# Optimization experiments

Hardware: AMD Instinct MI355X
Metric: run time of the kernel (lower is better)

## Reference

```python
import jax, jax.numpy as jnp
import numpy as np
from jax import lax

KS = 7  # kernel-prediction footprint at 1/4 res
DN = ('NCHW', 'OIHW', 'NCHW')


def _conv(x, W, b):
    y = lax.conv_general_dilated(x, W, (1, 1), 'VALID', dimension_numbers=DN)
    return y + b[None, :, None, None]


def _apply_kernels(kernel, data, ks):
    # kernel: [bs, ks*ks, kh, kw]; data: [bs, 1, h, w]
    kh, kw = kernel.shape[2], kernel.shape[3]
    h, w = data.shape[2], data.shape[3]
    ch = (h - (kh + ks - 1)) // 2
    cw = (w - (kw + ks - 1)) // 2
    if ch > 0:
        data = data[:, :, ch:h - ch, :]
    if cw > 0:
        data = data[:, :, :, cw:w - cw]
    # patches: [bs, ks*ks, kh, kw], flat tap index = dy*ks+dx (row-major), same as torch unfold+view
    patches = lax.conv_general_dilated_patches(data, (ks, ks), (1, 1), 'VALID')
    return jnp.sum(kernel * patches, axis=1, keepdims=True)


def _crop_like(a, b):
    dh = (a.shape[2] - b.shape[2]) // 2
    dw = (a.shape[3] - b.shape[3]) // 2
    if dh > 0 or dw > 0:
        a = a[:, :, dh:a.shape[2] - dh, dw:a.shape[3] - dw]
    return a


def _unroll(buf):
    # [bs,4,h,w] quarter-res -> [bs,1,2h,2w] full-res (channel c=2p+q -> offset (p,q))
    bs, _, h, w = buf.shape
    return buf.reshape(bs, 2, 2, h, w).transpose(0, 3, 1, 4, 2).reshape(bs, 1, 2 * h, 2 * w)


def reference(mosaic, W0, b0, W1, b1, W2, b2, W3, b3, W4, b4):
    gray = mosaic.sum(axis=1)  # [bs,H,W]
    # GRBG 2x2 phase extraction, matching torch unfold(2,2,2).unfold(1,2,2).permute(0,3,4,1,2)
    g0 = gray[:, 0::2, 0::2][:, None]
    b_ = gray[:, 1::2, 0::2][:, None]
    r = gray[:, 0::2, 1::2][:, None]
    g1 = gray[:, 1::2, 1::2][:, None]
    x = jnp.concatenate([g0, b_, r, g1], axis=1)  # [bs,4,h,w]

    # ConvChain: 5 valid 3x3 convs, relu on all but last (linear output)
    for (W, bb) in ((W0, b0), (W1, b1), (W2, b2), (W3, b3)):
        x = jax.nn.relu(_conv(x, W, bb))
    kernels = _conv(x, W4, b4)  # [bs, 10*KS*KS, kh, kw]

    k2 = KS * KS
    idx = 0

    reds = [r]
    for _ in range(3):
        k = jax.nn.softmax(kernels[:, idx:idx + k2], axis=1)
        idx += k2
        reds.append(_apply_kernels(k, r, KS))
    reds[0] = _crop_like(reds[0], reds[1])
    red = _unroll(jnp.concatenate([reds[1], reds[0], reds[2], reds[3]], axis=1))

    blues = [b_]
    for _ in range(3):
        k = jax.nn.softmax(kernels[:, idx:idx + k2], axis=1)
        idx += k2
        blues.append(_apply_kernels(k, b_, KS))
    blues[0] = _crop_like(blues[0], blues[1])
    blue = _unroll(jnp.concatenate([blues[1], blues[2], blues[0], blues[3]], axis=1))

    greens = [g0, g1]
    for _ in range(2):
        k = jax.nn.softmax(kernels[:, idx:idx + 2 * k2], axis=1)
        idx += 2 * k2
        greens.append(_apply_kernels(k[:, :k2], g0, KS) + _apply_kernels(k[:, k2:], g1, KS))
    greens[0] = _crop_like(greens[0], greens[2])
    greens[1] = _crop_like(greens[1], greens[2])
    green = _unroll(jnp.concatenate([greens[0], greens[2], greens[3], greens[1]], axis=1))

    return jnp.concatenate([red, green, blue], axis=1)  # [bs,3,2*kh,2*kw]


def setup_inputs() -> dict:
    key = jax.random.key(0)
    ks = jax.random.split(key, 6)
    bs, H, W = 2, 768, 768
    mosaic = jax.random.uniform(ks[0], (bs, 3, H, W), dtype=jnp.float32)

    def w(k, o, i):
        return jax.random.normal(k, (o, i, 3, 3), jnp.float32) * (1.0 / np.sqrt(i * 9))

    z = lambda n: jnp.zeros((n,), jnp.float32)
    return {
        'mosaic': mosaic,
        'W0': w(ks[1], 64, 4), 'b0': z(64),
        'W1': w(ks[2], 64, 64), 'b1': z(64),
        'W2': w(ks[3], 64, 64), 'b2': z(64),
        'W3': w(ks[4], 64, 64), 'b3': z(64),
        'W4': w(ks[5], 490, 64), 'b4': z(490),
    }
```

## Files before the change

kernel.cpp:

```cpp
#include <hip/hip_runtime.h>
#include <hip/hip_bf16.h>
#include <math.h>


typedef __attribute__((ext_vector_type(8))) short short8;
typedef __attribute__((ext_vector_type(4))) short short4v;
typedef __attribute__((ext_vector_type(4))) float f32x4;

static __device__ __forceinline__ short f2bf(float v) {
    __bf16 h = (__bf16)v;
    return __builtin_bit_cast(short, h);
}

__global__ __launch_bounds__(256) void split_k(const float* __restrict__ mosaic,
                                               float* __restrict__ x0) {
    int idx = blockIdx.x * 256 + threadIdx.x;
    const int total = 2 * 4 * 384 * 384;
    if (idx >= total) return;
    int x = idx % 384;
    int t = idx / 384;
    int y = t % 384;  t /= 384;
    int c = t % 4;
    int b = t / 4;
    int Y = 2 * y + ((c == 1 || c == 3) ? 1 : 0);
    int X = 2 * x + ((c == 2 || c == 3) ? 1 : 0);
    const float* mb = mosaic + (size_t)b * 3 * 768 * 768;
    float g = mb[Y * 768 + X] + mb[768 * 768 + Y * 768 + X] + mb[2 * 768 * 768 + Y * 768 + X];
    x0[idx] = g;
}

__global__ __launch_bounds__(256) void repack_k(const float* __restrict__ W,
                                                short* __restrict__ dst) {
    int idx = blockIdx.x * 256 + threadIdx.x;
    if (idx >= 9 * 64 * 64) return;
    int ic = idx % 64;
    int t2 = idx / 64;
    int oc = t2 % 64;
    int t  = t2 / 64;
    dst[idx] = f2bf(W[((size_t)oc * 64 + ic) * 9 + t]);
}

__global__ __launch_bounds__(256) void repack4_k(const float* __restrict__ W4,
                                                 const float* __restrict__ b4,
                                                 short* __restrict__ Wq,
                                                 float* __restrict__ bq) {
    int idx = blockIdx.x * 256 + threadIdx.x;
    if (idx < 9 * 640 * 64) {
        int ic  = idx % 64;
        int t2  = idx / 64;
        int ocn = t2 % 640;
        int tap = t2 / 640;
        int k  = ocn >> 6;
        int ql = ocn & 63;
        float v = (ql < 49) ? W4[((size_t)(49 * k + ql) * 64 + ic) * 9 + tap] : 0.f;
        Wq[idx] = f2bf(v);
    }
    if (idx < 640) {
        int k = idx >> 6, ql = idx & 63;
        bq[idx] = (ql < 49) ? b4[49 * k + ql] : 0.f;
    }
}

__global__ __launch_bounds__(256) void conv0_k(const float* __restrict__ x0f,
                                               const float* __restrict__ W0,
                                               const float* __restrict__ b0,
                                               short* __restrict__ out) {
    __shared__ float w[64 * 36];
    __shared__ float bb[64];
    for (int e = threadIdx.x; e < 64 * 36; e += 256) w[e] = W0[e];
    if (threadIdx.x < 64) bb[threadIdx.x] = b0[threadIdx.x];
    __syncthreads();
    int idx = blockIdx.x * 256 + threadIdx.x;
    if (idx >= 2 * 382 * 382) return;
    int x = idx % 382;
    int t = idx / 382;
    int y = t % 382;
    int b = t / 382;
    const float* base = x0f + (size_t)b * 4 * 384 * 384;
    float in[4][9];
#pragma unroll
    for (int ic = 0; ic < 4; ++ic)
#pragma unroll
        for (int ky = 0; ky < 3; ++ky)
#pragma unroll
            for (int kx = 0; kx < 3; ++kx)
                in[ic][ky * 3 + kx] = base[ic * 384 * 384 + (y + ky) * 384 + (x + kx)];
    short* op = out + (((size_t)b * 382 + y) * 382 + x) * 64;
    float accs[8];
    for (int og = 0; og < 8; ++og) {
#pragma unroll
        for (int oo = 0; oo < 8; ++oo) {
            int oc = og * 8 + oo;
            float acc = bb[oc];
            const float* wp = w + oc * 36;
#pragma unroll
            for (int ic = 0; ic < 4; ++ic)
#pragma unroll
                for (int e = 0; e < 9; ++e)
                    acc = fmaf(in[ic][e], wp[ic * 9 + e], acc);
            accs[oo] = fmaxf(acc, 0.f);
        }
        short8 pk;
#pragma unroll
        for (int oo = 0; oo < 8; ++oo) pk[oo] = f2bf(accs[oo]);
        *(short8*)(op + og * 8) = pk;
    }
}

template <int EPI>
__global__ __launch_bounds__(256, 2) void convp_k(
    const short* __restrict__ act,
    int Hin, int Hout, int YITER, int nstrips,
    const short* __restrict__ Wq,
    int CoutT,
    const float* __restrict__ bias,
    short* __restrict__ outbf,
    const float* __restrict__ x0f,
    float* __restrict__ out,
    float* __restrict__ pM, float* __restrict__ pD, float* __restrict__ pN) {
    const int tid = threadIdx.x;
    const int wave = tid >> 6;
    const int lane = tid & 63;
    const int wr = wave >> 1, wc = wave & 1;
    const int l15 = lane & 15, l4 = lane >> 4;

    const int q8 = gridDim.x >> 3;
    int L = ((int)blockIdx.x & 7) * q8 + ((int)blockIdx.x >> 3);
    int z = 0;
    if (EPI) { z = L % 10; L /= 10; }
    const int xt = L % 6; L /= 6;
    const int strip = L % nstrips;
    const int b = L / nstrips;
    const int x0c = xt * 64;
    const int y0 = strip * YITER;
    const int cnt = min(YITER, Hout - y0);
    if (cnt <= 0) return;

    __shared__ __align__(16) short Bt[4 * 528 * 8];
    __shared__ float smM[2][64], smD[2][64], smN[2][64];

    auto stage_row = [&](int r) {
        const size_t rowbase = ((size_t)b * Hin + r) * (size_t)Hin;
        const int ring = (r & 3) * 528;
#pragma unroll
        for (int i = 0; i < 2; ++i) {
            int s = i * 256 + tid;
            int xl = s >> 3, sl = s & 7;
            int gx = x0c + xl; if (gx > Hin - 1) gx = Hin - 1;
            const short* src = act + (rowbase + gx) * 64 + ((sl ^ (xl & 7)) << 3);
            __builtin_amdgcn_global_load_lds(
                (const __attribute__((address_space(1))) void*)src,
                (__attribute__((address_space(3))) void*)((char*)Bt + (ring + s) * 16),
                16, 0, 0);
        }
        if (tid < 16) {
            int s = 512 + tid;
            int xl = s >> 3, sl = s & 7;
            int gx = x0c + xl; if (gx > Hin - 1) gx = Hin - 1;
            const short* src = act + (rowbase + gx) * 64 + ((sl ^ (xl & 7)) << 3);
            __builtin_amdgcn_global_load_lds(
                (const __attribute__((address_space(1))) void*)src,
                (__attribute__((address_space(3))) void*)((char*)Bt + (ring + s) * 16),
                16, 0, 0);
        }
    };

    const int zrow = EPI ? z * 64 : 0;
    short8 wreg[9][2][2];
#pragma unroll
    for (int tap = 0; tap < 9; ++tap)
#pragma unroll
        for (int kk = 0; kk < 2; ++kk)
#pragma unroll
            for (int m = 0; m < 2; ++m)
                wreg[tap][kk][m] = *(const short8*)(Wq +
                    ((size_t)tap * CoutT + zrow + wr * 32 + m * 16 + l15) * 64
                    + kk * 32 + l4 * 8);

    float bv[2][4];
    int goff[2][4];
    const float* plane = nullptr;
    if (EPI) {
        int pidx = (z < 3) ? 2 : (z < 6) ? 1 : ((z & 1) ? 3 : 0);
        plane = x0f + ((size_t)b * 4 + pidx) * 384 * 384;
#pragma unroll
        for (int m = 0; m < 2; ++m)
#pragma unroll
            for (int r = 0; r < 4; ++r) {
                int q = wr * 32 + m * 16 + l4 * 4 + r;
                bv[m][r] = (q < 49) ? bias[z * 64 + q] : -1e30f;
                int qc = (q < 49) ? q : 48;
                goff[m][r] = (qc / 7) * 384 + (qc % 7);
            }
    }

    stage_row(y0);
    stage_row(y0 + 1);
    stage_row(y0 + 2);
    __syncthreads();

    for (int i = 0; i < cnt; ++i) {
        const int y = y0 + i;
        if (i <= cnt - 2) stage_row(y + 3);

        f32x4 acc[2][2] = {};
#pragma unroll
        for (int tap = 0; tap < 9; ++tap) {
            const int ky = tap / 3, kx = tap % 3;
            const int rbase = ((y + ky) & 3) * 528;
            short8 bf[2][2];
#pragma unroll
            for (int kk = 0; kk < 2; ++kk)
#pragma unroll
                for (int n = 0; n < 2; ++n) {
                    int xl = wc * 32 + n * 16 + l15 + kx;
                    int slot = (kk * 4 + l4) ^ (xl & 7);
                    bf[kk][n] = *(const short8*)&Bt[(rbase + xl * 8 + slot) * 8];
                }
#pragma unroll
            for (int kk = 0; kk < 2; ++kk)
#pragma unroll
                for (int m = 0; m < 2; ++m)
#pragma unroll
                    for (int n = 0; n < 2; ++n)
                        acc[m][n] = __builtin_amdgcn_mfma_f32_16x16x32_bf16(
                            wreg[tap][kk][m], bf[kk][n], acc[m][n], 0, 0, 0);
        }

        if (!EPI) {
#pragma unroll
            for (int m = 0; m < 2; ++m) {
                int ocb = wr * 32 + m * 16 + l4 * 4;
#pragma unroll
                for (int n = 0; n < 2; ++n) {
                    int x = x0c + wc * 32 + n * 16 + l15;
                    if (x >= Hout) continue;
                    size_t off = (((size_t)b * Hout + y) * Hout + x) * 64 + ocb;
                    short4v pk;
#pragma unroll
                    for (int r = 0; r < 4; ++r)
                        pk[r] = f2bf(fmaxf(acc[m][n][r] + bias[ocb + r], 0.f));
                    *(short4v*)(outbf + off) = pk;
                }
            }
            __syncthreads();
        } else {
            const float* gb = plane + (y + 2) * 384 + 2;
#pragma unroll
            for (int n = 0; n < 2; ++n) {
                const int xn = x0c + wc * 32 + n * 16 + l15;
                const int xg = (xn < 374) ? xn : 373;
                float mx = -1e30f;
#pragma unroll
                for (int m = 0; m < 2; ++m)
#pragma unroll
                    for (int r = 0; r < 4; ++r)
                        mx = fmaxf(mx, acc[m][n][r] + bv[m][r]);
                mx = fmaxf(mx, __shfl_xor(mx, 16));
                mx = fmaxf(mx, __shfl_xor(mx, 32));
                float den = 0.f, num = 0.f;
#pragma unroll
                for (int m = 0; m < 2; ++m)
#pragma unroll
                    for (int r = 0; r < 4; ++r) {
                        float e = __expf(acc[m][n][r] + bv[m][r] - mx);
                        den += e;
                        num = fmaf(e, gb[xg + goff[m][r]], num);
                    }
                den += __shfl_xor(den, 16);  den += __shfl_xor(den, 32);
                num += __shfl_xor(num, 16);  num += __shfl_xor(num, 32);
                if (l4 == 0) {
                    int p = wc * 32 + n * 16 + l15;
                    smM[wr][p] = mx;
                    smD[wr][p] = den;
                    smN[wr][p] = num;
                }
            }
            __syncthreads();
            if (tid < 64) {
                int p = tid, x = x0c + p;
                if (x < 374) {
                    float m0 = smM[0][p], m1 = smM[1][p];
                    float M = fmaxf(m0, m1);
                    float s0 = __expf(m0 - M), s1 = __expf(m1 - M);
                    float D = smD[0][p] * s0 + smD[1][p] * s1;
                    float N = smN[0][p] * s0 + smN[1][p] * s1;
                    if (z < 6) {
                        int color = (z < 3) ? 0 : 2;
                        int oy, ox;
                        switch (z) {
                            case 0: oy = 0; ox = 0; break;
                            case 1: oy = 1; ox = 0; break;
                            case 2: oy = 1; ox = 1; break;
                            case 3: oy = 0; ox = 0; break;
                            case 4: oy = 0; ox = 1; break;
                            default: oy = 1; ox = 1; break;
                        }
                        out[(((size_t)b * 3 + color) * 748 + 2 * y + oy) * 748 + 2 * x + ox] = N / D;
                    } else {
                        size_t po = (((size_t)(z - 6) * 2 + b) * 374 + y) * 374 + x;
                        pM[po] = M; pD[po] = D; pN[po] = N;
                    }
                }
            }
            __syncthreads();
        }
    }
}

__global__ __launch_bounds__(256) void rawcomb_k(
    const float* __restrict__ x0f,
    const float* __restrict__ pM, const float* __restrict__ pD,
    const float* __restrict__ pN,
    float* __restrict__ out) {
    int idx = blockIdx.x * 256 + threadIdx.x;
    if (idx >= 2 * 374 * 374) return;
    int x = idx % 374;
    int t = idx / 374;
    int y = t % 374;
    int b = t / 374;
    const float* pb = x0f + (size_t)b * 4 * 384 * 384;
    float* ob = out + (size_t)b * 3 * 748 * 748;
    float g0v = pb[(y + 5) * 384 + x + 5];
    float blv = pb[384 * 384 + (y + 5) * 384 + x + 5];
    float rrv = pb[2 * 384 * 384 + (y + 5) * 384 + x + 5];
    float g1v = pb[3 * 384 * 384 + (y + 5) * 384 + x + 5];
    ob[((size_t)0 * 748 + 2 * y) * 748 + 2 * x + 1]     = rrv;
    ob[((size_t)2 * 748 + 2 * y + 1) * 748 + 2 * x]     = blv;
    ob[((size_t)1 * 748 + 2 * y) * 748 + 2 * x]         = g0v;
    ob[((size_t)1 * 748 + 2 * y + 1) * 748 + 2 * x + 1] = g1v;
#pragma unroll
    for (int g = 0; g < 2; ++g) {
        size_t o0 = (((size_t)(g * 2 + 0) * 2 + b) * 374 + y) * 374 + x;
        size_t o1 = (((size_t)(g * 2 + 1) * 2 + b) * 374 + y) * 374 + x;
        float m0 = pM[o0], m1 = pM[o1];
        float M = fmaxf(m0, m1);
        float s0 = __expf(m0 - M), s1 = __expf(m1 - M);
        float val = (pN[o0] * s0 + pN[o1] * s1) / (pD[o0] * s0 + pD[o1] * s1);
        int oy = g ? 1 : 0, ox = g ? 0 : 1;
        ob[((size_t)1 * 748 + 2 * y + oy) * 748 + 2 * x + ox] = val;
    }
}

extern "C" void kernel_launch(void* const* d_in, const int* in_sizes, int n_in,
                              void* d_out, int out_size, void* d_ws, size_t ws_size,
                              hipStream_t stream) {
    const float* mosaic = (const float*)d_in[0];
    const float* W0 = (const float*)d_in[1];  const float* b0 = (const float*)d_in[2];
    const float* W1 = (const float*)d_in[3];  const float* b1 = (const float*)d_in[4];
    const float* W2 = (const float*)d_in[5];  const float* b2 = (const float*)d_in[6];
    const float* W3 = (const float*)d_in[7];  const float* b3 = (const float*)d_in[8];
    const float* W4 = (const float*)d_in[9];  const float* b4 = (const float*)d_in[10];
    float* out = (float*)d_out;

    char* ws = (char*)d_ws;
    float* x0f    = (float*)ws;  ws += 4718592;
    short* Wq1    = (short*)ws;  ws += 73728;
    short* Wq2    = (short*)ws;  ws += 73728;
    short* Wq3    = (short*)ws;  ws += 73728;
    short* Wq4p   = (short*)ws;  ws += 737280;
    float* bias4p = (float*)ws;  ws += 2560;
    short* bufA   = (short*)ws;  ws += 37356544;
    short* bufB   = (short*)ws;  ws += 36966400;
    float* pM     = (float*)ws;  ws += 4477568;
    float* pD     = (float*)ws;  ws += 4477568;
    float* pN     = (float*)ws;

    split_k<<<(2 * 4 * 384 * 384 + 255) / 256, 256, 0, stream>>>(mosaic, x0f);

    repack_k<<<(9 * 64 * 64 + 255) / 256, 256, 0, stream>>>(W1, Wq1);
    repack_k<<<(9 * 64 * 64 + 255) / 256, 256, 0, stream>>>(W2, Wq2);
    repack_k<<<(9 * 64 * 64 + 255) / 256, 256, 0, stream>>>(W3, Wq3);
    repack4_k<<<(9 * 640 * 64 + 255) / 256, 256, 0, stream>>>(W4, b4, Wq4p, bias4p);

    conv0_k<<<(2 * 382 * 382 + 255) / 256, 256, 0, stream>>>(x0f, W0, b0, bufA);

    convp_k<0><<<456, 256, 0, stream>>>(bufA, 382, 380, 10, 38, Wq1, 64, b1,
                                        bufB, nullptr, nullptr, nullptr, nullptr, nullptr);
    convp_k<0><<<456, 256, 0, stream>>>(bufB, 380, 378, 10, 38, Wq2, 64, b2,
                                        bufA, nullptr, nullptr, nullptr, nullptr, nullptr);
    convp_k<0><<<456, 256, 0, stream>>>(bufA, 378, 376, 10, 38, Wq3, 64, b3,
                                        bufB, nullptr, nullptr, nullptr, nullptr, nullptr);

    convp_k<1><<<4080, 256, 0, stream>>>(bufB, 376, 374, 11, 34, Wq4p, 640, bias4p,
                                         nullptr, x0f, out, pM, pD, pN);

    rawcomb_k<<<(2 * 374 * 374 + 255) / 256, 256, 0, stream>>>(x0f, pM, pD, pN, out);
}
```

Before: 467.2 us.

## Reuse each staged input row across three output rows with rotating accumulators

Restructures the row-sliding conv loop so each staged input row's B fragments are read from LDS once and fed into three in-flight accumulators (for output rows y, y-1, y-2), rotating accumulator roles across iterations. This cuts LDS reads per output row by about a factor of three and removes one barrier per row. It also retunes the grid decomposition (rows per block and block counts) for both the hidden convs and the kernel-prediction conv. The cost is three sets of accumulators held live in registers, a two-row pipeline warm-up per block, and extra control flow.

```diff
diff --git a/kernel.cpp b/kernel.cpp
--- a/kernel.cpp
+++ b/kernel.cpp
@@ -194,39 +194,7 @@
             }
     }
 
-    stage_row(y0);
-    stage_row(y0 + 1);
-    stage_row(y0 + 2);
-    __syncthreads();
-
-    for (int i = 0; i < cnt; ++i) {
-        const int y = y0 + i;
-        if (i <= cnt - 2) stage_row(y + 3);
-
-        f32x4 acc[2][2] = {};
-#pragma unroll
-        for (int tap = 0; tap < 9; ++tap) {
-            const int ky = tap / 3, kx = tap % 3;
-            const int rbase = ((y + ky) & 3) * 528;
-            short8 bf[2][2];
-#pragma unroll
-            for (int kk = 0; kk < 2; ++kk)
-#pragma unroll
-                for (int n = 0; n < 2; ++n) {
-                    int xl = wc * 32 + n * 16 + l15 + kx;
-                    int slot = (kk * 4 + l4) ^ (xl & 7);
-                    bf[kk][n] = *(const short8*)&Bt[(rbase + xl * 8 + slot) * 8];
-                }
-#pragma unroll
-            for (int kk = 0; kk < 2; ++kk)
-#pragma unroll
-                for (int m = 0; m < 2; ++m)
-#pragma unroll
-                    for (int n = 0; n < 2; ++n)
-                        acc[m][n] = __builtin_amdgcn_mfma_f32_16x16x32_bf16(
-                            wreg[tap][kk][m], bf[kk][n], acc[m][n], 0, 0, 0);
-        }
-
+    auto flush = [&](int orow, f32x4 (&ac)[2][2]) {
         if (!EPI) {
 #pragma unroll
             for (int m = 0; m < 2; ++m) {
@@ -235,17 +203,16 @@
                 for (int n = 0; n < 2; ++n) {
                     int x = x0c + wc * 32 + n * 16 + l15;
                     if (x >= Hout) continue;
-                    size_t off = (((size_t)b * Hout + y) * Hout + x) * 64 + ocb;
+                    size_t off = (((size_t)b * Hout + orow) * Hout + x) * 64 + ocb;
                     short4v pk;
 #pragma unroll
                     for (int r = 0; r < 4; ++r)
-                        pk[r] = f2bf(fmaxf(acc[m][n][r] + bias[ocb + r], 0.f));
+                        pk[r] = f2bf(fmaxf(ac[m][n][r] + bias[ocb + r], 0.f));
                     *(short4v*)(outbf + off) = pk;
                 }
             }
-            __syncthreads();
         } else {
-            const float* gb = plane + (y + 2) * 384 + 2;
+            const float* gb = plane + (orow + 2) * 384 + 2;
 #pragma unroll
             for (int n = 0; n < 2; ++n) {
                 const int xn = x0c + wc * 32 + n * 16 + l15;
@@ -255,7 +222,7 @@
                 for (int m = 0; m < 2; ++m)
 #pragma unroll
                     for (int r = 0; r < 4; ++r)
-                        mx = fmaxf(mx, acc[m][n][r] + bv[m][r]);
+                        mx = fmaxf(mx, ac[m][n][r] + bv[m][r]);
                 mx = fmaxf(mx, __shfl_xor(mx, 16));
                 mx = fmaxf(mx, __shfl_xor(mx, 32));
                 float den = 0.f, num = 0.f;
@@ -263,7 +230,7 @@
                 for (int m = 0; m < 2; ++m)
 #pragma unroll
                     for (int r = 0; r < 4; ++r) {
-                        float e = __expf(acc[m][n][r] + bv[m][r] - mx);
+                        float e = __expf(ac[m][n][r] + bv[m][r] - mx);
                         den += e;
                         num = fmaf(e, gb[xg + goff[m][r]], num);
                     }
@@ -296,16 +263,88 @@
                             case 4: oy = 0; ox = 1; break;
                             default: oy = 1; ox = 1; break;
                         }
-                        out[(((size_t)b * 3 + color) * 748 + 2 * y + oy) * 748 + 2 * x + ox] = N / D;
+                        out[(((size_t)b * 3 + color) * 748 + 2 * orow + oy) * 748 + 2 * x + ox] = N / D;
                     } else {
-                        size_t po = (((size_t)(z - 6) * 2 + b) * 374 + y) * 374 + x;
+                        size_t po = (((size_t)(z - 6) * 2 + b) * 374 + orow) * 374 + x;
                         pM[po] = M; pD[po] = D; pN[po] = N;
                     }
                 }
             }
-            __syncthreads();
         }
-    }
+    };
+
+    f32x4 aA[2][2] = {}, aB[2][2] = {}, aC[2][2] = {};
+
+    stage_row(y0);
+    stage_row(y0 + 1);
+    stage_row(y0 + 2);
+    __syncthreads();
+
+#define CONV_ITER(J, A0, A1, A2)                                              \
+    if ((J) < cnt + 2) {                                                      \
+        const int j_ = (J);                                                   \
+        const int r_ = y0 + j_;                                               \
+        if (j_ + 3 <= cnt + 1) stage_row(r_ + 3);                             \
+        const int rbase_ = (r_ & 3) * 528;                                    \
+        _Pragma("unroll")                                                     \
+        for (int kk = 0; kk < 2; ++kk) {                                      \
+            short8 bfk[3][2];                                                 \
+            _Pragma("unroll")                                                 \
+            for (int kx = 0; kx < 3; ++kx)                                    \
+                _Pragma("unroll")                                             \
+                for (int n = 0; n < 2; ++n) {                                 \
+                    int xl = wc * 32 + n * 16 + l15 + kx;                     \
+                    int slot = (kk * 4 + l4) ^ (xl & 7);                      \
+                    bfk[kx][n] = *(const short8*)&Bt[(rbase_ + xl * 8 + slot) * 8]; \
+                }                                                             \
+            if (j_ < cnt) {                                                   \
+                _Pragma("unroll")                                             \
+                for (int kx = 0; kx < 3; ++kx)                                \
+                    _Pragma("unroll")                                         \
+                    for (int m = 0; m < 2; ++m)                               \
+                        _Pragma("unroll")                                     \
+                        for (int n = 0; n < 2; ++n)                           \
+                            A0[m][n] = __builtin_amdgcn_mfma_f32_16x16x32_bf16( \
+                                wreg[kx][kk][m], bfk[kx][n], A0[m][n], 0, 0, 0); \
+            }                                                                 \
+            if (j_ >= 1 && j_ <= cnt) {                                       \
+                _Pragma("unroll")                                             \
+                for (int kx = 0; kx < 3; ++kx)                                \
+                    _Pragma("unroll")                                         \
+                    for (int m = 0; m < 2; ++m)                               \
+                        _Pragma("unroll")                                     \
+                        for (int n = 0; n < 2; ++n)                           \
+                            A1[m][n] = __builtin_amdgcn_mfma_f32_16x16x32_bf16( \
+                                wreg[3 + kx][kk][m], bfk[kx][n], A1[m][n], 0, 0, 0); \
+            }                                                                 \
+            if (j_ >= 2) {                                                    \
+                _Pragma("unroll")                                             \
+                for (int kx = 0; kx < 3; ++kx)                                \
+                    _Pragma("unroll")                                         \
+                    for (int m = 0; m < 2; ++m)                               \
+                        _Pragma("unroll")                                     \
+                        for (int n = 0; n < 2; ++n)                           \
+                            A2[m][n] = __builtin_amdgcn_mfma_f32_16x16x32_bf16( \
+                                wreg[6 + kx][kk][m], bfk[kx][n], A2[m][n], 0, 0, 0); \
+            }                                                                 \
+        }                                                                     \
+        if (j_ >= 2) {                                                        \
+            flush(y0 + j_ - 2, A2);                                           \
+            _Pragma("unroll")                                                 \
+            for (int m = 0; m < 2; ++m)                                       \
+                _Pragma("unroll")                                             \
+                for (int n = 0; n < 2; ++n)                                   \
+                    A2[m][n] = (f32x4){0.f, 0.f, 0.f, 0.f};                   \
+        }                                                                     \
+        __syncthreads();                                                      \
+    }
+
+    for (int jb = 0; jb < cnt + 2; jb += 3) {
+        CONV_ITER(jb + 0, aA, aC, aB)
+        CONV_ITER(jb + 1, aB, aA, aC)
+        CONV_ITER(jb + 2, aC, aB, aA)
+    }
+#undef CONV_ITER
 }
 
 __global__ __launch_bounds__(256) void rawcomb_k(
@@ -375,15 +414,15 @@
 
     conv0_k<<<(2 * 382 * 382 + 255) / 256, 256, 0, stream>>>(x0f, W0, b0, bufA);
 
-    convp_k<0><<<456, 256, 0, stream>>>(bufA, 382, 380, 10, 38, Wq1, 64, b1,
+    convp_k<0><<<576, 256, 0, stream>>>(bufA, 382, 380, 8, 48, Wq1, 64, b1,
                                         bufB, nullptr, nullptr, nullptr, nullptr, nullptr);
-    convp_k<0><<<456, 256, 0, stream>>>(bufB, 380, 378, 10, 38, Wq2, 64, b2,
+    convp_k<0><<<576, 256, 0, stream>>>(bufB, 380, 378, 8, 48, Wq2, 64, b2,
                                         bufA, nullptr, nullptr, nullptr, nullptr, nullptr);
-    convp_k<0><<<456, 256, 0, stream>>>(bufA, 378, 376, 10, 38, Wq3, 64, b3,
+    convp_k<0><<<576, 256, 0, stream>>>(bufA, 378, 376, 8, 48, Wq3, 64, b3,
                                         bufB, nullptr, nullptr, nullptr, nullptr, nullptr);
 
-    convp_k<1><<<4080, 256, 0, stream>>>(bufB, 376, 374, 11, 34, Wq4p, 640, bias4p,
-                                         nullptr, x0f, out, pM, pD, pN);
+    convp_k<1><<<960, 256, 0, stream>>>(bufB, 376, 374, 47, 8, Wq4p, 640, bias4p,
+                                        nullptr, x0f, out, pM, pD, pN);
 
     rawcomb_k<<<(2 * 374 * 374 + 255) / 256, 256, 0, stream>>>(x0f, pM, pD, pN, out);
 }
```

Result: slower. 1.037 ms (+121.9%).
